# Optimization experiments

Hardware: AMD Instinct MI355X
Metric: run time of the kernel (lower is better)

Reference implementation:

```python
import jax, jax.numpy as jnp
import numpy as np

H_DIM = 256
N_HEADS = 8
HALF = H_DIM // 2

def _lin(x, W, b):
    # torch nn.Linear: y = x @ W.T + b
    y = x @ W.T
    return y + b if b is not None else y

def setup_inputs() -> dict:
    key = jax.random.key(0)
    ks = jax.random.split(key, 16)
    s = 0.02
    d = {
        'x': jax.random.normal(ks[0], (16, H_DIM, 32, 32), jnp.float32),
        'q1_w': jax.random.normal(ks[1], (HALF, HALF), jnp.float32) * s,
        'q1_b': jnp.zeros((HALF,), jnp.float32),
        'q2_w': jax.random.normal(ks[2], (HALF, HALF), jnp.float32) * s,
        'q2_b': jnp.zeros((HALF,), jnp.float32),
        'k1_w': jax.random.normal(ks[3], (HALF, HALF), jnp.float32) * s,
        'k1_b': jnp.zeros((HALF,), jnp.float32),
        'k2_w': jax.random.normal(ks[4], (HALF, HALF), jnp.float32) * s,
        'k2_b': jnp.zeros((HALF,), jnp.float32),
        'v1_w': jax.random.normal(ks[5], (HALF, HALF), jnp.float32) * s,
        'v1_b': jnp.zeros((HALF,), jnp.float32),
        'v2_w': jax.random.normal(ks[6], (HALF, HALF), jnp.float32) * s,
        'v2_b': jnp.zeros((HALF,), jnp.float32),
        'proj1_w': jax.random.normal(ks[7], (HALF, HALF), jnp.float32) * s,
        'proj1_b': jnp.zeros((HALF,), jnp.float32),
        'proj2_w': jax.random.normal(ks[8], (HALF, HALF), jnp.float32) * s,
        'proj2_b': jnp.zeros((HALF,), jnp.float32),
        'logit_scale': jnp.log(10.0 * jnp.ones((N_HEADS, 1, 1), jnp.float32)),
        'mlp_w1': jax.random.normal(ks[9], (128, 2), jnp.float32) * s,
        'mlp_b1': jnp.zeros((128,), jnp.float32),
        'mlp_w2': jax.random.normal(ks[10], (N_HEADS, 128), jnp.float32) * s,
    }
    return d

def _rel_pos_index(h, w):
    # static (numpy) relative position index, shape [N, N]
    ch, cw = np.meshgrid(np.arange(h), np.arange(w), indexing='ij')
    coords = np.stack([ch.reshape(-1), cw.reshape(-1)])  # [2, N]
    rel = coords[:, :, None] - coords[:, None, :]         # [2, N, N]
    rel = rel.transpose(1, 2, 0)
    rel[:, :, 0] += h - 1
    rel[:, :, 1] += w - 1
    return rel[:, :, 0] * (2 * w - 1) + rel[:, :, 1]

def _forward(x, q1_w, q1_b, q2_w, q2_b, k1_w, k1_b, k2_w, k2_b,
             v1_w, v1_b, v2_w, v2_b, proj1_w, proj1_b, proj2_w, proj2_b,
             logit_scale, mlp_w1, mlp_b1, mlp_w2):
    b, c, h, w = x.shape
    N = h * w
    nh = N_HEADS
    hd = c // nh
    x3 = jnp.transpose(x, (0, 2, 3, 1)).reshape(b, N, c)
    x0, x1 = x3[..., :c // 2], x3[..., c // 2:]

    def qkv(W0, b0, W1, b1):
        t = jnp.concatenate([x0 + _lin(x0, W0, b0), x1 + _lin(x1, W1, b1)], axis=-1)
        return t.reshape(b, N, nh, hd).transpose(0, 2, 1, 3)  # [b, nh, N, hd]

    q = qkv(q1_w, q1_b, q2_w, q2_b)
    k = qkv(k1_w, k1_b, k2_w, k2_b)
    v = qkv(v1_w, v1_b, v2_w, v2_b)

    eps = 1e-12
    qn = q / jnp.maximum(jnp.linalg.norm(q, axis=-1, keepdims=True), eps)
    kn = k / jnp.maximum(jnp.linalg.norm(k, axis=-1, keepdims=True), eps)
    attn = jnp.einsum('bhnd,bhmd->bhnm', qn, kn)  # cosine similarity
    scale = jnp.exp(jnp.minimum(logit_scale, jnp.log(1.0 / 0.01)))  # [nh,1,1]
    attn = attn * scale[None]

    # continuous relative-position bias (CPB) table via small MLP
    rch = jnp.arange(-(h - 1), h, dtype=jnp.float32) / (h - 1 + 1e-8)
    rcw = jnp.arange(-(w - 1), w, dtype=jnp.float32) / (w - 1 + 1e-8)
    gh, gw = jnp.meshgrid(rch, rcw, indexing='ij')
    tab = jnp.stack([gh, gw], axis=-1) * 3.2               # [2h-1, 2w-1, 2]
    tab = jnp.sign(tab) * (1.0 - jnp.exp(-jnp.abs(tab)))
    tab = jax.nn.relu(_lin(tab, mlp_w1, mlp_b1))
    tab = _lin(tab, mlp_w2, None).reshape(-1, nh)          # [(2h-1)(2w-1), nh]

    idx = jnp.asarray(_rel_pos_index(h, w))                # [N, N]
    bias = tab[idx.reshape(-1)].reshape(N, N, nh).transpose(2, 0, 1)
    bias = 16.0 * jax.nn.sigmoid(bias)
    attn = attn + bias[None]

    attn = jax.nn.softmax(attn, axis=-1)
    out = jnp.einsum('bhnm,bhmd->bhnd', attn, v).transpose(0, 2, 1, 3).reshape(b, N, c)
    o0, o1 = out[..., :c // 2], out[..., c // 2:]
    out = jnp.concatenate([_lin(o0, proj1_w, proj1_b), _lin(o1, proj2_w, proj2_b)], axis=-1)
    return out.reshape(b, h, w, c).transpose(0, 3, 1, 2)

def reference(x, q1_w, q1_b, q2_w, q2_b, k1_w, k1_b, k2_w, k2_b,
              v1_w, v1_b, v2_w, v2_b, proj1_w, proj1_b, proj2_w, proj2_b,
              logit_scale, mlp_w1, mlp_b1, mlp_w2):
    return _forward(x, q1_w, q1_b, q2_w, q2_b, k1_w, k1_b, k2_w, k2_b,
                    v1_w, v1_b, v2_w, v2_b, proj1_w, proj1_b, proj2_w, proj2_b,
                    logit_scale, mlp_w1, mlp_b1, mlp_w2)
```

## Files before the change

kernel.cpp:

```cpp
#include <hip/hip_runtime.h>
#include <cmath>


typedef _Float16 half_t;
typedef __attribute__((ext_vector_type(2))) __fp16 fp16x2;
typedef __attribute__((ext_vector_type(4))) _Float16 half4;
typedef __attribute__((ext_vector_type(8))) _Float16 half8;
typedef __attribute__((ext_vector_type(2))) float float2v;
typedef __attribute__((ext_vector_type(4))) float float4v;
typedef __attribute__((ext_vector_type(4))) unsigned int uint4v;

static __device__ __forceinline__ float4v mfma16(half8 a, half8 b, float4v c) {
  return __builtin_amdgcn_mfma_f32_16x16x32_f16(a, b, c, 0, 0, 0);
}

struct PtrArr8 { const float* p[8]; };

__global__ __launch_bounds__(256) void prep_w(PtrArr8 wsrc, PtrArr8 bsrc,
                                              half_t* __restrict__ wf,
                                              float* __restrict__ bws) {
  int y = blockIdx.y;
  const float* src = nullptr;
  const float* bs = nullptr;
#pragma unroll
  for (int i = 0; i < 8; i++)
    if (i == y) { src = wsrc.p[i]; bs = bsrc.p[i]; }
  int flat = (blockIdx.x * 256 + threadIdx.x) * 4;
  float4 w = *(const float4*)(src + flat);
  int j = flat >> 7, k = flat & 127;
  if (y < 6) {
    if (k == j)     w.x += 1.0f;
    if (k + 1 == j) w.y += 1.0f;
    if (k + 2 == j) w.z += 1.0f;
    if (k + 3 == j) w.w += 1.0f;
  }
  half4 h;
  h[0] = (half_t)w.x;
  h[1] = (half_t)w.y;
  h[2] = (half_t)w.z;
  h[3] = (half_t)w.w;
  int ng = j >> 4, l = j & 15, ks = k >> 5, quad = (k >> 3) & 3, o8 = k & 7;
  *(half4*)(wf + y * 16384 + ((ng * 4 + ks) * 64 + quad * 16 + l) * 8 + o8) =
      h;
  if (blockIdx.x == 0 && threadIdx.x < 128)
    bws[y * 128 + threadIdx.x] = bs[threadIdx.x];
}

__global__ __launch_bounds__(256) void bias_mlp(const float* __restrict__ w1,
                                                const float* __restrict__ b1,
                                                const float* __restrict__ w2,
                                                const float* __restrict__ ls,
                                                float* __restrict__ tabh2) {
  __shared__ float sw1[256];
  __shared__ float sb1[128];
  __shared__ float sw2[1024];
  int t = threadIdx.x;
  sw1[t] = w1[t];
  if (t < 128) sb1[t] = b1[t];
  for (int i = t; i < 1024; i += 256) sw2[i] = w2[i];
  __syncthreads();
  int p = blockIdx.x * 256 + t;
  if (p >= 3969) return;
  int ph = p / 63, pw = p % 63;
  float t0 = (float)(ph - 31) * (3.2f / 31.0f);
  float t1 = (float)(pw - 31) * (3.2f / 31.0f);
  t0 = copysignf(1.0f - __expf(-fabsf(t0)), t0);
  t1 = copysignf(1.0f - __expf(-fabsf(t1)), t1);
  float acc[8];
#pragma unroll
  for (int hh = 0; hh < 8; hh++) acc[hh] = 0.0f;
  for (int j = 0; j < 128; j++) {
    float hj = fmaxf(0.0f, t0 * sw1[2 * j] + t1 * sw1[2 * j + 1] + sb1[j]);
#pragma unroll
    for (int hh = 0; hh < 8; hh++) acc[hh] += hj * sw2[hh * 128 + j];
  }
  const float L2E = 1.44269504f;
#pragma unroll
  for (int hh = 0; hh < 8; hh++) {
    float scale = __expf(fminf(ls[hh], 4.6051702f));
    float c14 = 14.0f - (scale + 16.0f) * L2E;
    float bias = 16.0f / (1.0f + __expf(-acc[hh]));
    tabh2[hh * 3969 + p] = bias * L2E + c14;
  }
}

__global__ __launch_bounds__(256, 4) void qkv_mfma(
    const float* __restrict__ x, const half_t* __restrict__ wfrag,
    const float* __restrict__ lscale, const float* __restrict__ bws,
    half_t* __restrict__ qf, half_t* __restrict__ kf,
    half_t* __restrict__ vf) {
  __shared__ half_t tbuf[4608];
  int t = threadIdx.x;
  int lane = t & 63, wv = t >> 6, l = lane & 15, quad = lane >> 4;
  int rw = wv & 1, cw = wv >> 1;
  int hf = blockIdx.y;
  int m0 = blockIdx.x * 32;
  int b = m0 >> 10, n0 = m0 & 1023;

  half8 afr[4];
  {
    const float* xb =
        x + ((size_t)b * 256 + hf * 128) * 1024 + n0 + rw * 16 + l;
#pragma unroll
    for (int ks = 0; ks < 4; ks++) {
      half8 a;
#pragma unroll
      for (int j = 0; j < 8; j++)
        a[j] = (half_t)xb[(size_t)(ks * 32 + quad * 8 + j) * 1024];
      afr[ks] = a;
    }
  }

  for (int op = 0; op < 3; op++) {
    int combo = op * 2 + hf;
    const half_t* wfb = wfrag + combo * 16384;
    float4v acc[4];
#pragma unroll
    for (int ngl = 0; ngl < 4; ngl++) {
      int ng = cw * 4 + ngl;
      float4v c = {0.f, 0.f, 0.f, 0.f};
#pragma unroll
      for (int ks = 0; ks < 4; ks++) {
        half8 bfrag =
            *(const half8*)(wfb + ((ng * 4 + ks) * 64 + lane) * 8);
        c = mfma16(afr[ks], bfrag, c);
      }
      acc[ngl] = c;
    }
#pragma unroll
    for (int ngl = 0; ngl < 4; ngl++) {
      float bb = bws[combo * 128 + (cw * 4 + ngl) * 16 + l];
#pragma unroll
      for (int r2 = 0; r2 < 4; r2++) acc[ngl][r2] += bb;
    }
    if (op < 2) {
#pragma unroll
      for (int hgl = 0; hgl < 2; hgl++) {
        float sc = 1.0f;
        if (op == 0)
          sc = __expf(fminf(lscale[hf * 4 + cw * 2 + hgl], 4.6051702f)) *
               1.44269504f;
#pragma unroll
        for (int r2 = 0; r2 < 4; r2++) {
          float ss = acc[2 * hgl][r2] * acc[2 * hgl][r2] +
                     acc[2 * hgl + 1][r2] * acc[2 * hgl + 1][r2];
          ss += __shfl_xor(ss, 1, 64);
          ss += __shfl_xor(ss, 2, 64);
          ss += __shfl_xor(ss, 4, 64);
          ss += __shfl_xor(ss, 8, 64);
          float rn = sc / fmaxf(sqrtf(ss), 1e-12f);
          acc[2 * hgl][r2] *= rn;
          acc[2 * hgl + 1][r2] *= rn;
        }
      }
#pragma unroll
      for (int ngl = 0; ngl < 4; ngl++)
#pragma unroll
        for (int r2 = 0; r2 < 4; r2++)
          tbuf[(rw * 16 + quad * 4 + r2) * 136 + (cw * 4 + ngl) * 16 + l] =
              (half_t)acc[ngl][r2];
      __syncthreads();
      half_t* dst = (op == 0) ? qf : kf;
#pragma unroll
      for (int i = 0; i < 2; i++) {
        int idx = t + 256 * i;
        int row = idx >> 4, colc = (idx & 15) * 8;
        half8 vv = *(const half8*)(tbuf + row * 136 + colc);
        int head = hf * 4 + (colc >> 5), d = colc & 31;
        *(half8*)(dst + (((size_t)b * 8 + head) * 1024 + n0 + row) * 32 + d) =
            vv;
      }
      __syncthreads();
    } else {
#pragma unroll
      for (int ngl = 0; ngl < 4; ngl++) {
        int col = (cw * 4 + ngl) * 16 + l;
        half4 hv;
#pragma unroll
        for (int r2 = 0; r2 < 4; r2++) hv[r2] = (half_t)acc[ngl][r2];
        *(half4*)(tbuf + col * 36 + rw * 16 + quad * 4) = hv;
      }
      __syncthreads();
      int p64 = (n0 >> 5) & 1;
      int nb64 = n0 & ~63;
#pragma unroll
      for (int i = 0; i < 8; i++) {
        int idx = t + 256 * i;
        int col = idx >> 4, rp = idx & 15;
        unsigned int val = *(const unsigned int*)(tbuf + col * 36 + rp * 2);
        int head = hf * 4 + (col >> 5);
        int d = col & 31;
        int npos = nb64 + ((rp >> 1) & 3) * 16 + (rp & 1) * 8 + p64 * 4 +
                   ((rp >> 3) & 1) * 2;
        *(unsigned int*)((char*)vf +
                         (((((size_t)b * 8 + head) * 32 + d) * 1024) + npos) *
                             2) = val;
      }
    }
  }
}


#define LOADK(kt)                                                           \
  {                                                                         \
    _Pragma("unroll") for (int nt = 0; nt < 4; nt++)                        \
        kfr[nt] = *(const half8*)(kbase + ((kt)*64 + nt * 16 + l) * 32 +    \
                                  quad * 8);                                \
  }

#define LOADV(kt)                                                           \
  {                                                                         \
    _Pragma("unroll") for (int ks = 0; ks < 2; ks++) {                      \
      vv0[ks] = *(const half8*)(vbase + l * 1024 + (kt)*64 + quad * 16 +    \
                                ks * 8);                                    \
      vv1[ks] = *(const half8*)(vbase + (16 + l) * 1024 + (kt)*64 +         \
                                quad * 16 + ks * 8);                        \
    }                                                                       \
  }

#define QK_PHASE(kt, S, SR)                                                 \
  {                                                                         \
    int rowb = (wv + 31 - 2 * (kt)) * 63 + cA + (S)*16;                     \
    _Pragma("unroll") for (int nt = 0; nt < 4; nt++) {                      \
      int base = rowb - (nt >> 1) * 63 - (nt & 1) * 16;                     \
      float2v p0 = sb2d[base];                                              \
      float2v p1 = sb2d[base - 2];                                          \
      float4v c;                                                            \
      c[0] = p0[1];                                                         \
      c[1] = p0[0];                                                         \
      c[2] = p1[1];                                                         \
      c[3] = p1[0];                                                         \
      SR[nt] = mfma16(kfr[nt], qfr[S], c);                                  \
    }                                                                       \
  }

#define EXP_PACK(S, SR)                                                     \
  {                                                                         \
    unsigned int w0[4], w1[4];                                              \
    _Pragma("unroll") for (int nt = 0; nt < 4; nt++) {                      \
      fp16x2 plo = __builtin_amdgcn_cvt_pkrtz(exp2f(SR[nt][0]),             \
                                              exp2f(SR[nt][1]));            \
      fp16x2 phi = __builtin_amdgcn_cvt_pkrtz(exp2f(SR[nt][2]),             \
                                              exp2f(SR[nt][3]));            \
      w0[nt] = __builtin_bit_cast(unsigned int, plo);                       \
      w1[nt] = __builtin_bit_cast(unsigned int, phi);                       \
    }                                                                       \
    uint4v u0 = {w0[0], w0[1], w0[2], w0[3]};                               \
    uint4v u1 = {w1[0], w1[1], w1[2], w1[3]};                               \
    pf##S[0] = __builtin_bit_cast(half8, u0);                               \
    pf##S[1] = __builtin_bit_cast(half8, u1);                               \
  }

#define PV_PHASE(S)                                                         \
  {                                                                         \
    _Pragma("unroll") for (int ks = 0; ks < 2; ks++) {                      \
      o0[S] = mfma16(pf##S[ks], vv0[ks], o0[S]);                            \
      o1[S] = mfma16(pf##S[ks], vv1[ks], o1[S]);                            \
      accl[S] = mfma16(pf##S[ks], ones, accl[S]);                           \
    }                                                                       \
  }

__global__ __launch_bounds__(256) void attn_mfma(
    const half_t* __restrict__ qf, const half_t* __restrict__ kf,
    const half_t* __restrict__ vf, const float* __restrict__ tabh2,
    half_t* __restrict__ ao) {
  __shared__ float2v sb2d[2205];

  int id = blockIdx.x;
  int qo = id >> 7;
  int bh = id & 127;
  int h = bh & 7, b = bh >> 3;
  int t = threadIdx.x;
  int lane = t & 63, wv = t >> 6, l = lane & 15, quad = lane >> 4;
  size_t bhs = (size_t)b * 8 + h;
  const half_t* kbase = kf + bhs * 1024 * 32;
  const half_t* vbase = vf + bhs * 32 * 1024;
  int row0 = qo * 128 + wv * 32;
  int cA = l + 31 - quad * 4;

  half8 kfr[4], vv0[2], vv1[2], qfr[2], pf0[2], pf1[2];
  LOADK(0);
  LOADV(0);
#pragma unroll
  for (int s = 0; s < 2; s++)
    qfr[s] = *(const half8*)(qf + (bhs * 1024 + row0 + s * 16 + l) * 32 +
                             quad * 8);

  {
    const float* tb = tabh2 + h * 3969 + qo * 252;
    for (int i = t; i < 2205; i += 256) {
      float2v pr;
      pr[0] = (i > 0) ? tb[i - 1] : 0.0f;
      pr[1] = tb[i];
      sb2d[i] = pr;
    }
  }

  float4v o0[2], o1[2], accl[2];
#pragma unroll
  for (int s = 0; s < 2; s++) {
    o0[s] = (float4v){0.f, 0.f, 0.f, 0.f};
    o1[s] = (float4v){0.f, 0.f, 0.f, 0.f};
    accl[s] = (float4v){0.f, 0.f, 0.f, 0.f};
  }
  half8 ones;
#pragma unroll
  for (int j = 0; j < 8; j++) ones[j] = (half_t)1.0f;

  __syncthreads();

#pragma unroll
  for (int kt = 0; kt < 16; ++kt) {
    float4v sres[4];
    QK_PHASE(kt, 0, sres);
    EXP_PACK(0, sres);
    float4v sres2[4];
    QK_PHASE(kt, 1, sres2);
    if (kt < 15) LOADK(kt + 1);
    EXP_PACK(1, sres2);
    PV_PHASE(0);
    PV_PHASE(1);
    if (kt < 15) LOADV(kt + 1);
  }

#pragma unroll
  for (int s = 0; s < 2; s++) {
#pragma unroll
    for (int r2 = 0; r2 < 4; r2++) {
      float linv = 1.0f / accl[s][r2];
      size_t rowaddr =
          ((size_t)b * 1024 + row0 + s * 16 + quad * 4 + r2) * 256 + h * 32;
      ao[rowaddr + l] = (half_t)(o0[s][r2] * linv);
      ao[rowaddr + 16 + l] = (half_t)(o1[s][r2] * linv);
    }
  }
}

__global__ __launch_bounds__(256, 4) void proj_mfma(
    const half_t* __restrict__ ao, const half_t* __restrict__ wfrag,
    const float* __restrict__ bws, float* __restrict__ out) {
  __shared__ float yt[128 * 36];
  int t = threadIdx.x;
  int lane = t & 63, wv = t >> 6, l = lane & 15, quad = lane >> 4;
  int rw = wv & 1, cw = wv >> 1;
  int hf = blockIdx.y;
  int m0 = blockIdx.x * 32;
  int b = m0 >> 10, n0 = m0 & 1023;

  half8 afr[4];
  const half_t* ab =
      ao + ((size_t)m0 + rw * 16 + l) * 256 + hf * 128 + quad * 8;
#pragma unroll
  for (int ks = 0; ks < 4; ks++) afr[ks] = *(const half8*)(ab + ks * 32);

  const half_t* wfb = wfrag + (6 + hf) * 16384;
#pragma unroll
  for (int ngl = 0; ngl < 4; ngl++) {
    int ng = cw * 4 + ngl;
    float4v c = {0.f, 0.f, 0.f, 0.f};
#pragma unroll
    for (int ks = 0; ks < 4; ks++) {
      half8 bfrag = *(const half8*)(wfb + ((ng * 4 + ks) * 64 + lane) * 8);
      c = mfma16(afr[ks], bfrag, c);
    }
    float bb = bws[(6 + hf) * 128 + ng * 16 + l];
#pragma unroll
    for (int r2 = 0; r2 < 4; r2++) c[r2] += bb;
    *(float4v*)(yt + (ng * 16 + l) * 36 + rw * 16 + quad * 4) = c;
  }
  __syncthreads();
#pragma unroll
  for (int i = 0; i < 4; i++) {
    int idx = t + 256 * i;
    int col = idx >> 3, rg = idx & 7;
    float4v vv = *(const float4v*)(yt + col * 36 + rg * 4);
    *(float4v*)(out + ((size_t)b * 256 + hf * 128 + col) * 1024 + n0 +
                rg * 4) = vv;
  }
}

extern "C" void kernel_launch(void* const* d_in, const int* in_sizes, int n_in,
                              void* d_out, int out_size, void* d_ws,
                              size_t ws_size, hipStream_t stream) {
  (void)in_sizes; (void)n_in; (void)out_size; (void)ws_size;
  const float* x = (const float*)d_in[0];

  half_t* ws = (half_t*)d_ws;
  half_t* qfp = ws;
  half_t* kfp = ws + 4194304;
  half_t* vfp = ws + 8388608;
  half_t* aop = ws + 12582912;
  half_t* wfp = ws + 16777216;
  float* tabh2 = (float*)((char*)d_ws + 33816576);
  float* bws = (float*)((char*)d_ws + 33943584);

  PtrArr8 wsrc, bsrc;
  const int widx[8] = {1, 3, 5, 7, 9, 11, 13, 15};
  for (int i = 0; i < 8; i++) {
    wsrc.p[i] = (const float*)d_in[widx[i]];
    bsrc.p[i] = (const float*)d_in[widx[i] + 1];
  }

  prep_w<<<dim3(16, 8), 256, 0, stream>>>(wsrc, bsrc, wfp, bws);
  bias_mlp<<<16, 256, 0, stream>>>((const float*)d_in[18],
                                   (const float*)d_in[19],
                                   (const float*)d_in[20],
                                   (const float*)d_in[17], tabh2);
  qkv_mfma<<<dim3(512, 2), 256, 0, stream>>>(x, wfp, (const float*)d_in[17],
                                             bws, qfp, kfp, vfp);
  attn_mfma<<<1024, 256, 0, stream>>>(qfp, kfp, vfp, tabh2, aop);
  proj_mfma<<<dim3(512, 2), 256, 0, stream>>>(aop, wfp, bws, (float*)d_out);
}
```

Measured before the change: 190.9 us.

## Halve attention rows per block and merge weight-prep and bias-MLP kernels

The attention kernel now has each wave handle one 16-row query tile instead of two, so a block covers 64 query rows and the grid doubles to 2048 blocks. The bias-table slice staged in shared memory shrinks to match. This trades per-wave instruction-level parallelism and doubled K/V re-reads for more blocks, less shared memory and fewer registers per wave, aiming at better occupancy and load balance. Separately, the weight-prep and relative-position-bias MLP kernels are fused into one launch, with blocks branching by index, to save a kernel launch.

```diff
diff --git a/kernel.cpp b/kernel.cpp
--- a/kernel.cpp
+++ b/kernel.cpp
@@ -16,71 +16,70 @@
 
 struct PtrArr8 { const float* p[8]; };
 
-__global__ __launch_bounds__(256) void prep_w(PtrArr8 wsrc, PtrArr8 bsrc,
-                                              half_t* __restrict__ wf,
-                                              float* __restrict__ bws) {
-  int y = blockIdx.y;
-  const float* src = nullptr;
-  const float* bs = nullptr;
-#pragma unroll
-  for (int i = 0; i < 8; i++)
-    if (i == y) { src = wsrc.p[i]; bs = bsrc.p[i]; }
-  int flat = (blockIdx.x * 256 + threadIdx.x) * 4;
-  float4 w = *(const float4*)(src + flat);
-  int j = flat >> 7, k = flat & 127;
-  if (y < 6) {
-    if (k == j)     w.x += 1.0f;
-    if (k + 1 == j) w.y += 1.0f;
-    if (k + 2 == j) w.z += 1.0f;
-    if (k + 3 == j) w.w += 1.0f;
-  }
-  half4 h;
-  h[0] = (half_t)w.x;
-  h[1] = (half_t)w.y;
-  h[2] = (half_t)w.z;
-  h[3] = (half_t)w.w;
-  int ng = j >> 4, l = j & 15, ks = k >> 5, quad = (k >> 3) & 3, o8 = k & 7;
-  *(half4*)(wf + y * 16384 + ((ng * 4 + ks) * 64 + quad * 16 + l) * 8 + o8) =
-      h;
-  if (blockIdx.x == 0 && threadIdx.x < 128)
-    bws[y * 128 + threadIdx.x] = bs[threadIdx.x];
-}
-
-__global__ __launch_bounds__(256) void bias_mlp(const float* __restrict__ w1,
-                                                const float* __restrict__ b1,
-                                                const float* __restrict__ w2,
-                                                const float* __restrict__ ls,
-                                                float* __restrict__ tabh2) {
-  __shared__ float sw1[256];
-  __shared__ float sb1[128];
-  __shared__ float sw2[1024];
+__global__ __launch_bounds__(256) void prep_all(
+    PtrArr8 wsrc, PtrArr8 bsrc, half_t* __restrict__ wf,
+    float* __restrict__ bws, const float* __restrict__ w1,
+    const float* __restrict__ b1, const float* __restrict__ w2,
+    const float* __restrict__ ls, float* __restrict__ tabh2) {
+  __shared__ float smem[1408];
+  int blk = blockIdx.x;
   int t = threadIdx.x;
-  sw1[t] = w1[t];
-  if (t < 128) sb1[t] = b1[t];
-  for (int i = t; i < 1024; i += 256) sw2[i] = w2[i];
-  __syncthreads();
-  int p = blockIdx.x * 256 + t;
-  if (p >= 3969) return;
-  int ph = p / 63, pw = p % 63;
-  float t0 = (float)(ph - 31) * (3.2f / 31.0f);
-  float t1 = (float)(pw - 31) * (3.2f / 31.0f);
-  t0 = copysignf(1.0f - __expf(-fabsf(t0)), t0);
-  t1 = copysignf(1.0f - __expf(-fabsf(t1)), t1);
-  float acc[8];
-#pragma unroll
-  for (int hh = 0; hh < 8; hh++) acc[hh] = 0.0f;
-  for (int j = 0; j < 128; j++) {
-    float hj = fmaxf(0.0f, t0 * sw1[2 * j] + t1 * sw1[2 * j + 1] + sb1[j]);
-#pragma unroll
-    for (int hh = 0; hh < 8; hh++) acc[hh] += hj * sw2[hh * 128 + j];
-  }
-  const float L2E = 1.44269504f;
-#pragma unroll
-  for (int hh = 0; hh < 8; hh++) {
-    float scale = __expf(fminf(ls[hh], 4.6051702f));
-    float c14 = 14.0f - (scale + 16.0f) * L2E;
-    float bias = 16.0f / (1.0f + __expf(-acc[hh]));
-    tabh2[hh * 3969 + p] = bias * L2E + c14;
+  if (blk < 128) {
+    int y = blk >> 4, xx = blk & 15;
+    const float* src = nullptr;
+    const float* bs = nullptr;
+#pragma unroll
+    for (int i = 0; i < 8; i++)
+      if (i == y) { src = wsrc.p[i]; bs = bsrc.p[i]; }
+    int flat = (xx * 256 + t) * 4;
+    float4 w = *(const float4*)(src + flat);
+    int j = flat >> 7, k = flat & 127;
+    if (y < 6) {
+      if (k == j)     w.x += 1.0f;
+      if (k + 1 == j) w.y += 1.0f;
+      if (k + 2 == j) w.z += 1.0f;
+      if (k + 3 == j) w.w += 1.0f;
+    }
+    half4 h;
+    h[0] = (half_t)w.x;
+    h[1] = (half_t)w.y;
+    h[2] = (half_t)w.z;
+    h[3] = (half_t)w.w;
+    int ng = j >> 4, l = j & 15, ks = k >> 5, quad = (k >> 3) & 3, o8 = k & 7;
+    *(half4*)(wf + y * 16384 + ((ng * 4 + ks) * 64 + quad * 16 + l) * 8 +
+              o8) = h;
+    if (xx == 0 && t < 128) bws[y * 128 + t] = bs[t];
+  } else {
+    float* sw1 = smem;
+    float* sb1 = smem + 256;
+    float* sw2 = smem + 384;
+    sw1[t] = w1[t];
+    if (t < 128) sb1[t] = b1[t];
+    for (int i = t; i < 1024; i += 256) sw2[i] = w2[i];
+    __syncthreads();
+    int p = (blk - 128) * 256 + t;
+    if (p >= 3969) return;
+    int ph = p / 63, pw = p % 63;
+    float t0 = (float)(ph - 31) * (3.2f / 31.0f);
+    float t1 = (float)(pw - 31) * (3.2f / 31.0f);
+    t0 = copysignf(1.0f - __expf(-fabsf(t0)), t0);
+    t1 = copysignf(1.0f - __expf(-fabsf(t1)), t1);
+    float acc[8];
+#pragma unroll
+    for (int hh = 0; hh < 8; hh++) acc[hh] = 0.0f;
+    for (int j = 0; j < 128; j++) {
+      float hj = fmaxf(0.0f, t0 * sw1[2 * j] + t1 * sw1[2 * j + 1] + sb1[j]);
+#pragma unroll
+      for (int hh = 0; hh < 8; hh++) acc[hh] += hj * sw2[hh * 128 + j];
+    }
+    const float L2E = 1.44269504f;
+#pragma unroll
+    for (int hh = 0; hh < 8; hh++) {
+      float scale = __expf(fminf(ls[hh], 4.6051702f));
+      float c14 = 14.0f - (scale + 16.0f) * L2E;
+      float bias = 16.0f / (1.0f + __expf(-acc[hh]));
+      tabh2[hh * 3969 + p] = bias * L2E + c14;
+    }
   }
 }
 
@@ -218,9 +217,9 @@
     }                                                                       \
   }
 
-#define QK_PHASE(kt, S, SR)                                                 \
-  {                                                                         \
-    int rowb = (wv + 31 - 2 * (kt)) * 63 + cA + (S)*16;                     \
+#define QK_PHASE(kt, SR)                                                    \
+  {                                                                         \
+    int rowb = (rA - 2 * (kt)) * 63 + cA;                                   \
     _Pragma("unroll") for (int nt = 0; nt < 4; nt++) {                      \
       int base = rowb - (nt >> 1) * 63 - (nt & 1) * 16;                     \
       float2v p0 = sb2d[base];                                              \
@@ -230,11 +229,11 @@
       c[1] = p0[0];                                                         \
       c[2] = p1[1];                                                         \
       c[3] = p1[0];                                                         \
-      SR[nt] = mfma16(kfr[nt], qfr[S], c);                                  \
+      SR[nt] = mfma16(kfr[nt], qfr, c);                                     \
     }                                                                       \
   }
 
-#define EXP_PACK(S, SR)                                                     \
+#define EXP_PACK(SR)                                                        \
   {                                                                         \
     unsigned int w0[4], w1[4];                                              \
     _Pragma("unroll") for (int nt = 0; nt < 4; nt++) {                      \
@@ -247,16 +246,16 @@
     }                                                                       \
     uint4v u0 = {w0[0], w0[1], w0[2], w0[3]};                               \
     uint4v u1 = {w1[0], w1[1], w1[2], w1[3]};                               \
-    pf##S[0] = __builtin_bit_cast(half8, u0);                               \
-    pf##S[1] = __builtin_bit_cast(half8, u1);                               \
-  }
-
-#define PV_PHASE(S)                                                         \
+    pf[0] = __builtin_bit_cast(half8, u0);                                  \
+    pf[1] = __builtin_bit_cast(half8, u1);                                  \
+  }
+
+#define PV_PHASE()                                                          \
   {                                                                         \
     _Pragma("unroll") for (int ks = 0; ks < 2; ks++) {                      \
-      o0[S] = mfma16(pf##S[ks], vv0[ks], o0[S]);                            \
-      o1[S] = mfma16(pf##S[ks], vv1[ks], o1[S]);                            \
-      accl[S] = mfma16(pf##S[ks], ones, accl[S]);                           \
+      o0 = mfma16(pf[ks], vv0[ks], o0);                                     \
+      o1 = mfma16(pf[ks], vv1[ks], o1);                                     \
+      accl = mfma16(pf[ks], ones, accl);                                    \
     }                                                                       \
   }
 
@@ -264,7 +263,7 @@
     const half_t* __restrict__ qf, const half_t* __restrict__ kf,
     const half_t* __restrict__ vf, const float* __restrict__ tabh2,
     half_t* __restrict__ ao) {
-  __shared__ float2v sb2d[2205];
+  __shared__ float2v sb2d[2079];
 
   int id = blockIdx.x;
   int qo = id >> 7;
@@ -275,20 +274,18 @@
   size_t bhs = (size_t)b * 8 + h;
   const half_t* kbase = kf + bhs * 1024 * 32;
   const half_t* vbase = vf + bhs * 32 * 1024;
-  int row0 = qo * 128 + wv * 32;
-  int cA = l + 31 - quad * 4;
-
-  half8 kfr[4], vv0[2], vv1[2], qfr[2], pf0[2], pf1[2];
+  int row0 = qo * 64 + wv * 16;
+  int rA = (wv >> 1) + 31;
+  int cA = (wv & 1) * 16 + l + 31 - quad * 4;
+
+  half8 kfr[4], vv0[2], vv1[2], qfr, pf[2];
   LOADK(0);
   LOADV(0);
-#pragma unroll
-  for (int s = 0; s < 2; s++)
-    qfr[s] = *(const half8*)(qf + (bhs * 1024 + row0 + s * 16 + l) * 32 +
-                             quad * 8);
+  qfr = *(const half8*)(qf + (bhs * 1024 + row0 + l) * 32 + quad * 8);
 
   {
-    const float* tb = tabh2 + h * 3969 + qo * 252;
-    for (int i = t; i < 2205; i += 256) {
+    const float* tb = tabh2 + h * 3969 + qo * 126;
+    for (int i = t; i < 2079; i += 256) {
       float2v pr;
       pr[0] = (i > 0) ? tb[i - 1] : 0.0f;
       pr[1] = tb[i];
@@ -296,13 +293,9 @@
     }
   }
 
-  float4v o0[2], o1[2], accl[2];
-#pragma unroll
-  for (int s = 0; s < 2; s++) {
-    o0[s] = (float4v){0.f, 0.f, 0.f, 0.f};
-    o1[s] = (float4v){0.f, 0.f, 0.f, 0.f};
-    accl[s] = (float4v){0.f, 0.f, 0.f, 0.f};
-  }
+  float4v o0 = {0.f, 0.f, 0.f, 0.f};
+  float4v o1 = {0.f, 0.f, 0.f, 0.f};
+  float4v accl = {0.f, 0.f, 0.f, 0.f};
   half8 ones;
 #pragma unroll
   for (int j = 0; j < 8; j++) ones[j] = (half_t)1.0f;
@@ -312,27 +305,20 @@
 #pragma unroll
   for (int kt = 0; kt < 16; ++kt) {
     float4v sres[4];
-    QK_PHASE(kt, 0, sres);
-    EXP_PACK(0, sres);
-    float4v sres2[4];
-    QK_PHASE(kt, 1, sres2);
+    QK_PHASE(kt, sres);
     if (kt < 15) LOADK(kt + 1);
-    EXP_PACK(1, sres2);
-    PV_PHASE(0);
-    PV_PHASE(1);
+    EXP_PACK(sres);
+    PV_PHASE();
     if (kt < 15) LOADV(kt + 1);
   }
 
 #pragma unroll
-  for (int s = 0; s < 2; s++) {
-#pragma unroll
-    for (int r2 = 0; r2 < 4; r2++) {
-      float linv = 1.0f / accl[s][r2];
-      size_t rowaddr =
-          ((size_t)b * 1024 + row0 + s * 16 + quad * 4 + r2) * 256 + h * 32;
-      ao[rowaddr + l] = (half_t)(o0[s][r2] * linv);
-      ao[rowaddr + 16 + l] = (half_t)(o1[s][r2] * linv);
-    }
+  for (int r2 = 0; r2 < 4; r2++) {
+    float linv = 1.0f / accl[r2];
+    size_t rowaddr =
+        ((size_t)b * 1024 + row0 + quad * 4 + r2) * 256 + h * 32;
+    ao[rowaddr + l] = (half_t)(o0[r2] * linv);
+    ao[rowaddr + 16 + l] = (half_t)(o1[r2] * linv);
   }
 }
 
@@ -401,13 +387,13 @@
     bsrc.p[i] = (const float*)d_in[widx[i] + 1];
   }
 
-  prep_w<<<dim3(16, 8), 256, 0, stream>>>(wsrc, bsrc, wfp, bws);
-  bias_mlp<<<16, 256, 0, stream>>>((const float*)d_in[18],
-                                   (const float*)d_in[19],
-                                   (const float*)d_in[20],
-                                   (const float*)d_in[17], tabh2);
+  prep_all<<<144, 256, 0, stream>>>(wsrc, bsrc, wfp, bws,
+                                    (const float*)d_in[18],
+                                    (const float*)d_in[19],
+                                    (const float*)d_in[20],
+                                    (const float*)d_in[17], tabh2);
   qkv_mfma<<<dim3(512, 2), 256, 0, stream>>>(x, wfp, (const float*)d_in[17],
                                              bws, qfp, kfp, vfp);
-  attn_mfma<<<1024, 256, 0, stream>>>(qfp, kfp, vfp, tabh2, aop);
+  attn_mfma<<<2048, 256, 0, stream>>>(qfp, kfp, vfp, tabh2, aop);
   proj_mfma<<<dim3(512, 2), 256, 0, stream>>>(aop, wfp, bws, (float*)d_out);
 }
```

Measured after the change: 225.4 us. 1.18x slower.
